# Kernel tuning notes

Measured on AMD Instinct MI355X. Metric: run time of the kernel, lower is better.

## Reference

```python
import jax, jax.numpy as jnp
import numpy as np

B, T, D, H, S = 32, 2048, 512, 64, 3  # batch, time, feature_dim, flow hidden, flow steps
NBLK = 2  # nflows MADE default num_blocks
LOG_2PI = np.float32(np.log(2.0 * np.pi))


def setup_inputs() -> dict:
    key = jax.random.key(0)
    ks = jax.random.split(key, 20)
    rn = lambda k, sh: jax.random.normal(k, sh, dtype=jnp.float32) * 0.05
    return {
        "trend": rn(ks[0], (B, T)),
        "seasonal": rn(ks[1], (B, T)),
        "residual": rn(ks[2], (B, T)),
        # Linear(1, D) for trend / seasonal
        "Wt": rn(ks[3], (D, 1)), "bt": rn(ks[4], (D,)),
        "Ws": rn(ks[5], (D, 1)), "bs": rn(ks[6], (D,)),
        # per-flow-step MADE params (stacked over S steps). With features=1 the
        # masked initial layer contributes only its bias.
        "b_init": rn(ks[7], (S, H)),
        "Wc0": rn(ks[8], (S, H, 1)), "bc0": rn(ks[9], (S, H)),
        # two residual blocks per step: lin1, lin2, context gate
        "W1": rn(ks[10], (S, NBLK, H, H)), "b1": rn(ks[11], (S, NBLK, H)),
        "W2": rn(ks[12], (S, NBLK, H, H)), "b2": rn(ks[13], (S, NBLK, H)),
        "Wcb": rn(ks[14], (S, NBLK, H, 1)), "bcb": rn(ks[15], (S, NBLK, H)),
        # final Linear(H, 2): (unconstrained_scale, shift)
        "Wf": rn(ks[16], (S, 2, H)), "bf": rn(ks[17], (S, 2)),
    }


def _flow_log_prob(x, c, b_init, Wc0, bc0, W1, b1, W2, b2, Wcb, bcb, Wf, bf):
    # x: [N] residual values, c: [N,1] context (previous residual)
    z = x
    logdet = jnp.zeros_like(x)
    for i in range(S):
        h = c @ Wc0[i].T + (bc0[i] + b_init[i])  # [N,H]; input path is fully masked (features=1)
        for j in range(NBLK):  # MaskedResidualBlock
            t = jax.nn.relu(h) @ W1[i, j].T + b1[i, j]
            t = jax.nn.relu(t) @ W2[i, j].T + b2[i, j]
            g = c @ Wcb[i, j].T + bcb[i, j]
            h = h + t * jax.nn.sigmoid(g)  # F.glu(cat(t, g))
        out = jax.nn.relu(h) @ Wf[i].T + bf[i]  # [N,2]
        scale = jax.nn.softplus(out[:, 0]) + 1e-3
        z = scale * z + out[:, 1]
        logdet = logdet + jnp.log(scale)
    return -0.5 * z * z - 0.5 * LOG_2PI + logdet  # StandardNormal.log_prob + logabsdet


def reference(trend, seasonal, residual, Wt, bt, Ws, bs, b_init, Wc0, bc0,
              W1, b1, W2, b2, Wcb, bcb, Wf, bf):
    # Linear(1, D): y = x * W[:,0] + b
    feat_trend = trend[..., None] * Wt[:, 0] + bt      # [B,T,D]
    feat_seasonal = seasonal[..., None] * Ws[:, 0] + bs  # [B,T,D]
    x = residual.reshape(-1)                            # [B*T]
    prev = jnp.concatenate([jnp.zeros_like(residual[:, :1]), residual[:, :-1]], axis=1)
    c = prev.reshape(-1, 1)                             # [B*T,1]
    lp = _flow_log_prob(x, c, b_init, Wc0, bc0, W1, b1, W2, b2, Wcb, bcb, Wf, bf)
    lp = jax.lax.stop_gradient(lp).reshape(B, T, 1)     # torch.no_grad()
    return jnp.concatenate([feat_trend, feat_seasonal, lp], axis=-1)  # [B,T,2D+1]
```

## Files before the change

kernel.cpp:

```cpp
#include <hip/hip_runtime.h>

#define NB 32
#define NT 2048
#define ND 512
#define NH 64
#define NS 3
#define NBLKS 2
#define ROWLEN (2*ND + 1)

typedef __attribute__((ext_vector_type(8))) short bf16x8;
typedef float f32x4 __attribute__((ext_vector_type(4)));

#define W1_OFF 0
#define W2_OFF 24576
#define WF_OFF 49152
#define WS_ELEMS 52224

__device__ __forceinline__ unsigned int f2bf(float f) {
    unsigned int u = __float_as_uint(f);
    return (u + 0x7FFFu + ((u >> 16) & 1u)) >> 16;
}
__device__ __forceinline__ unsigned int pack2(float a, float b) {
    return f2bf(a) | (f2bf(b) << 16);
}

__global__ __launch_bounds__(256) void prepack(
    const float* __restrict__ W1, const float* __restrict__ W2,
    const float* __restrict__ Wf, unsigned short* __restrict__ ws)
{
    int idx = blockIdx.x * 256 + threadIdx.x;
    if (idx < 24576) {
        ws[W1_OFF + idx] = (unsigned short)f2bf(W1[idx]);
    } else if (idx < 49152) {
        int o = idx - 24576;
        ws[W2_OFF + o] = (unsigned short)f2bf(W2[o]);
    } else if (idx < WS_ELEMS) {
        int o = idx - 49152;
        int s = o >> 10, row = (o >> 6) & 15, m = o & 63;
        float v = (row < 2) ? Wf[s * 128 + row * 64 + m] : 0.0f;
        ws[WF_OFF + o] = (unsigned short)f2bf(v);
    }
}

__global__ __launch_bounds__(256, 4) void nf_main(
    const float* __restrict__ trend, const float* __restrict__ seasonal,
    const float* __restrict__ residual,
    const float* __restrict__ Wt, const float* __restrict__ bt,
    const float* __restrict__ Ws, const float* __restrict__ bs,
    const float* __restrict__ b_init, const float* __restrict__ Wc0,
    const float* __restrict__ bc0,
    const float* __restrict__ b1, const float* __restrict__ b2,
    const float* __restrict__ Wcb, const float* __restrict__ bcb,
    const float* __restrict__ bf_, const unsigned short* __restrict__ wpk,
    float* __restrict__ out)
{
    __shared__ float s_tr[64], s_se[64];
    __shared__ unsigned short s_X[4][16][72];

    const int tid  = threadIdx.x;
    const int row0 = blockIdx.x * 64;

    if (tid < 64) { s_tr[tid] = trend[row0 + tid]; s_se[tid] = seasonal[row0 + tid]; }
    __syncthreads();

    {
        float wv[4], bv[4];
        #pragma unroll
        for (int j = 0; j < 4; ++j) {
            int cc = tid + 256 * j;
            if (cc < ND) { wv[j] = Wt[cc];      bv[j] = bt[cc]; }
            else         { wv[j] = Ws[cc - ND]; bv[j] = bs[cc - ND]; }
        }
        for (int rr = 0; rr < 64; ++rr) {
            float a = s_tr[rr], sv = s_se[rr];
            float* rp = out + (size_t)(row0 + rr) * ROWLEN;
            #pragma unroll
            for (int j = 0; j < 4; ++j) {
                int cc = tid + 256 * j;
                rp[cc] = fmaf((cc < ND) ? a : sv, wv[j], bv[j]);
            }
        }
    }

    const int lane = tid & 63;
    const int wv_  = tid >> 6;
    const int r    = lane & 15;
    const int q    = lane >> 4;
    const int n    = row0 + wv_ * 16 + r;
    const float x  = residual[n];
    const float c  = ((n & (NT - 1)) == 0) ? 0.0f : residual[n - 1];
    unsigned short (* const X)[72] = s_X[wv_];
    const int u0 = 4 * q;

    float z = x, logdet = 0.0f;

    for (int i = 0; i < NS; ++i) {
        float h[4][4];
        #pragma unroll
        for (int t = 0; t < 4; ++t) {
            const int ub = i * NH + 16 * t + u0;
            const f32x4 wc  = *(const f32x4*)(Wc0 + ub);
            const f32x4 b0v = *(const f32x4*)(bc0 + ub);
            const f32x4 biv = *(const f32x4*)(b_init + ub);
            #pragma unroll
            for (int e = 0; e < 4; ++e) h[t][e] = fmaf(c, wc[e], b0v[e] + biv[e]);
        }

        for (int j = 0; j < NBLKS; ++j) {
            const int ij = i * NBLKS + j;
            #pragma unroll
            for (int t = 0; t < 4; ++t) {
                uint2 p;
                p.x = pack2(fmaxf(h[t][0], 0.f), fmaxf(h[t][1], 0.f));
                p.y = pack2(fmaxf(h[t][2], 0.f), fmaxf(h[t][3], 0.f));
                *(uint2*)&X[r][16 * t + u0] = p;
            }
            __syncthreads();

            f32x4 D[4];
            {
                const unsigned short* Wb = wpk + W1_OFF + ij * 4096;
                bf16x8 bA = *(const bf16x8*)&X[r][8 * q];
                bf16x8 bB = *(const bf16x8*)&X[r][32 + 8 * q];
                #pragma unroll
                for (int t = 0; t < 4; ++t) {
                    bf16x8 a0 = *(const bf16x8*)&Wb[(16 * t + r) * 64 + 8 * q];
                    bf16x8 a1 = *(const bf16x8*)&Wb[(16 * t + r) * 64 + 32 + 8 * q];
                    f32x4 d = {0.f, 0.f, 0.f, 0.f};
                    d = __builtin_amdgcn_mfma_f32_16x16x32_bf16(a0, bA, d, 0, 0, 0);
                    d = __builtin_amdgcn_mfma_f32_16x16x32_bf16(a1, bB, d, 0, 0, 0);
                    D[t] = d;
                }
            }
            #pragma unroll
            for (int t = 0; t < 4; ++t) {
                const f32x4 bb = *(const f32x4*)(b1 + ij * NH + 16 * t + u0);
                uint2 p;
                p.x = pack2(fmaxf(D[t][0] + bb[0], 0.f), fmaxf(D[t][1] + bb[1], 0.f));
                p.y = pack2(fmaxf(D[t][2] + bb[2], 0.f), fmaxf(D[t][3] + bb[3], 0.f));
                *(uint2*)&X[r][16 * t + u0] = p;
            }
            __syncthreads();

            {
                const unsigned short* Wb = wpk + W2_OFF + ij * 4096;
                bf16x8 bA = *(const bf16x8*)&X[r][8 * q];
                bf16x8 bB = *(const bf16x8*)&X[r][32 + 8 * q];
                #pragma unroll
                for (int t = 0; t < 4; ++t) {
                    bf16x8 a0 = *(const bf16x8*)&Wb[(16 * t + r) * 64 + 8 * q];
                    bf16x8 a1 = *(const bf16x8*)&Wb[(16 * t + r) * 64 + 32 + 8 * q];
                    f32x4 d = {0.f, 0.f, 0.f, 0.f};
                    d = __builtin_amdgcn_mfma_f32_16x16x32_bf16(a0, bA, d, 0, 0, 0);
                    d = __builtin_amdgcn_mfma_f32_16x16x32_bf16(a1, bB, d, 0, 0, 0);
                    D[t] = d;
                }
            }
            #pragma unroll
            for (int t = 0; t < 4; ++t) {
                const int ub = ij * NH + 16 * t + u0;
                const f32x4 b2v = *(const f32x4*)(b2 + ub);
                const f32x4 wg  = *(const f32x4*)(Wcb + ub);
                const f32x4 bg  = *(const f32x4*)(bcb + ub);
                #pragma unroll
                for (int e = 0; e < 4; ++e) {
                    float g  = fmaf(c, wg[e], bg[e]);
                    float sg = 1.0f / (1.0f + __expf(-g));
                    h[t][e] += (D[t][e] + b2v[e]) * sg;
                }
            }
        }

        #pragma unroll
        for (int t = 0; t < 4; ++t) {
            uint2 p;
            p.x = pack2(fmaxf(h[t][0], 0.f), fmaxf(h[t][1], 0.f));
            p.y = pack2(fmaxf(h[t][2], 0.f), fmaxf(h[t][3], 0.f));
            *(uint2*)&X[r][16 * t + u0] = p;
        }
        __syncthreads();
        {
            const unsigned short* Wb = wpk + WF_OFF + i * 1024;
            bf16x8 bA = *(const bf16x8*)&X[r][8 * q];
            bf16x8 bB = *(const bf16x8*)&X[r][32 + 8 * q];
            bf16x8 a0 = *(const bf16x8*)&Wb[r * 64 + 8 * q];
            bf16x8 a1 = *(const bf16x8*)&Wb[r * 64 + 32 + 8 * q];
            f32x4 d = {0.f, 0.f, 0.f, 0.f};
            d = __builtin_amdgcn_mfma_f32_16x16x32_bf16(a0, bA, d, 0, 0, 0);
            d = __builtin_amdgcn_mfma_f32_16x16x32_bf16(a1, bB, d, 0, 0, 0);
            float o0 = d[0] + bf_[2 * i];
            float o1 = d[1] + bf_[2 * i + 1];
            float sp = log1pf(__expf(o0)) + 1e-3f;
            z = fmaf(sp, z, o1);
            logdet += __logf(sp);
        }
        __syncthreads();
    }

    if (q == 0)
        out[(size_t)n * ROWLEN + 2 * ND] = fmaf(-0.5f, z * z, logdet) - 0.91893853320467274178f;
}

extern "C" void kernel_launch(void* const* d_in, const int* in_sizes, int n_in,
                              void* d_out, int out_size, void* d_ws, size_t ws_size,
                              hipStream_t stream) {
    const float* trend    = (const float*)d_in[0];
    const float* seasonal = (const float*)d_in[1];
    const float* residual = (const float*)d_in[2];
    const float* Wt       = (const float*)d_in[3];
    const float* bt       = (const float*)d_in[4];
    const float* Ws       = (const float*)d_in[5];
    const float* bs       = (const float*)d_in[6];
    const float* b_init   = (const float*)d_in[7];
    const float* Wc0      = (const float*)d_in[8];
    const float* bc0      = (const float*)d_in[9];
    const float* W1       = (const float*)d_in[10];
    const float* b1       = (const float*)d_in[11];
    const float* W2       = (const float*)d_in[12];
    const float* b2       = (const float*)d_in[13];
    const float* Wcb      = (const float*)d_in[14];
    const float* bcb      = (const float*)d_in[15];
    const float* Wf       = (const float*)d_in[16];
    const float* bfin     = (const float*)d_in[17];
    float* out            = (float*)d_out;
    unsigned short* wpk   = (unsigned short*)d_ws;

    hipLaunchKernelGGL(prepack, dim3(WS_ELEMS / 256), dim3(256), 0, stream, W1, W2, Wf, wpk);

    const int nrows = NB * NT;
    hipLaunchKernelGGL(nf_main, dim3(nrows / 64), dim3(256), 0, stream,
                       trend, seasonal, residual, Wt, bt, Ws, bs,
                       b_init, Wc0, bc0, b1, b2, Wcb, bcb, bfin, wpk, out);
}
```

Before: 354.3 us.

## Keep MFMA activations in registers via permuted weight rows, drop LDS round-trips

Prepack now permutes the output-unit order of W1 and W2 so that each MFMA's output fragment lands in exactly the lanes and positions the next MFMA needs as its B operand. The activations can then be packed to bf16 directly in registers instead of being written to shared memory and read back. This removes the LDS staging buffer and every __syncthreads in the flow loop, and it also unrolls the block loop. The cost is a more intricate index mapping that must exactly match the MFMA fragment layout, or results will be silently wrong.

```diff
diff --git a/kernel.cpp b/kernel.cpp
--- a/kernel.cpp
+++ b/kernel.cpp
@@ -24,16 +24,22 @@
     return f2bf(a) | (f2bf(b) << 16);
 }
 
+__device__ __forceinline__ int uperm(int s) {
+    return (((s >> 2) & 3) << 3) + (((s >> 4) & 1) << 2) + (s & 3) + ((s >> 5) << 5);
+}
+
 __global__ __launch_bounds__(256) void prepack(
     const float* __restrict__ W1, const float* __restrict__ W2,
     const float* __restrict__ Wf, unsigned short* __restrict__ ws)
 {
     int idx = blockIdx.x * 256 + threadIdx.x;
     if (idx < 24576) {
-        ws[W1_OFF + idx] = (unsigned short)f2bf(W1[idx]);
+        int mat = idx >> 12, s = (idx >> 6) & 63, k = idx & 63;
+        ws[W1_OFF + idx] = (unsigned short)f2bf(W1[(mat << 12) + uperm(s) * 64 + k]);
     } else if (idx < 49152) {
         int o = idx - 24576;
-        ws[W2_OFF + o] = (unsigned short)f2bf(W2[o]);
+        int mat = o >> 12, s = (o >> 6) & 63, k = o & 63;
+        ws[W2_OFF + o] = (unsigned short)f2bf(W2[(mat << 12) + uperm(s) * 64 + k]);
     } else if (idx < WS_ELEMS) {
         int o = idx - 49152;
         int s = o >> 10, row = (o >> 6) & 15, m = o & 63;
@@ -55,7 +61,6 @@
     float* __restrict__ out)
 {
     __shared__ float s_tr[64], s_se[64];
-    __shared__ unsigned short s_X[4][16][72];
 
     const int tid  = threadIdx.x;
     const int row0 = blockIdx.x * 64;
@@ -89,8 +94,11 @@
     const int n    = row0 + wv_ * 16 + r;
     const float x  = residual[n];
     const float c  = ((n & (NT - 1)) == 0) ? 0.0f : residual[n - 1];
-    unsigned short (* const X)[72] = s_X[wv_];
-    const int u0 = 4 * q;
+
+    const int pb0 = 8 * q;
+    const int pbt[4] = {pb0, pb0 + 4, pb0 + 32, pb0 + 36};
+
+    union B8 { unsigned int u[4]; bf16x8 v; };
 
     float z = x, logdet = 0.0f;
 
@@ -98,7 +106,7 @@
         float h[4][4];
         #pragma unroll
         for (int t = 0; t < 4; ++t) {
-            const int ub = i * NH + 16 * t + u0;
+            const int ub = i * NH + pbt[t];
             const f32x4 wc  = *(const f32x4*)(Wc0 + ub);
             const f32x4 b0v = *(const f32x4*)(bc0 + ub);
             const f32x4 biv = *(const f32x4*)(b_init + ub);
@@ -106,59 +114,66 @@
             for (int e = 0; e < 4; ++e) h[t][e] = fmaf(c, wc[e], b0v[e] + biv[e]);
         }
 
+        #pragma unroll
         for (int j = 0; j < NBLKS; ++j) {
             const int ij = i * NBLKS + j;
-            #pragma unroll
-            for (int t = 0; t < 4; ++t) {
-                uint2 p;
-                p.x = pack2(fmaxf(h[t][0], 0.f), fmaxf(h[t][1], 0.f));
-                p.y = pack2(fmaxf(h[t][2], 0.f), fmaxf(h[t][3], 0.f));
-                *(uint2*)&X[r][16 * t + u0] = p;
-            }
-            __syncthreads();
+
+            B8 bA, bB;
+            bA.u[0] = pack2(fmaxf(h[0][0], 0.f), fmaxf(h[0][1], 0.f));
+            bA.u[1] = pack2(fmaxf(h[0][2], 0.f), fmaxf(h[0][3], 0.f));
+            bA.u[2] = pack2(fmaxf(h[1][0], 0.f), fmaxf(h[1][1], 0.f));
+            bA.u[3] = pack2(fmaxf(h[1][2], 0.f), fmaxf(h[1][3], 0.f));
+            bB.u[0] = pack2(fmaxf(h[2][0], 0.f), fmaxf(h[2][1], 0.f));
+            bB.u[1] = pack2(fmaxf(h[2][2], 0.f), fmaxf(h[2][3], 0.f));
+            bB.u[2] = pack2(fmaxf(h[3][0], 0.f), fmaxf(h[3][1], 0.f));
+            bB.u[3] = pack2(fmaxf(h[3][2], 0.f), fmaxf(h[3][3], 0.f));
 
             f32x4 D[4];
             {
                 const unsigned short* Wb = wpk + W1_OFF + ij * 4096;
-                bf16x8 bA = *(const bf16x8*)&X[r][8 * q];
-                bf16x8 bB = *(const bf16x8*)&X[r][32 + 8 * q];
                 #pragma unroll
                 for (int t = 0; t < 4; ++t) {
                     bf16x8 a0 = *(const bf16x8*)&Wb[(16 * t + r) * 64 + 8 * q];
                     bf16x8 a1 = *(const bf16x8*)&Wb[(16 * t + r) * 64 + 32 + 8 * q];
                     f32x4 d = {0.f, 0.f, 0.f, 0.f};
-                    d = __builtin_amdgcn_mfma_f32_16x16x32_bf16(a0, bA, d, 0, 0, 0);
-                    d = __builtin_amdgcn_mfma_f32_16x16x32_bf16(a1, bB, d, 0, 0, 0);
+                    d = __builtin_amdgcn_mfma_f32_16x16x32_bf16(a0, bA.v, d, 0, 0, 0);
+                    d = __builtin_amdgcn_mfma_f32_16x16x32_bf16(a1, bB.v, d, 0, 0, 0);
                     D[t] = d;
                 }
             }
-            #pragma unroll
-            for (int t = 0; t < 4; ++t) {
-                const f32x4 bb = *(const f32x4*)(b1 + ij * NH + 16 * t + u0);
-                uint2 p;
-                p.x = pack2(fmaxf(D[t][0] + bb[0], 0.f), fmaxf(D[t][1] + bb[1], 0.f));
-                p.y = pack2(fmaxf(D[t][2] + bb[2], 0.f), fmaxf(D[t][3] + bb[3], 0.f));
-                *(uint2*)&X[r][16 * t + u0] = p;
-            }
-            __syncthreads();
+
+            B8 cA, cB;
+            {
+                const f32x4 c0 = *(const f32x4*)(b1 + ij * NH + pbt[0]);
+                const f32x4 c1 = *(const f32x4*)(b1 + ij * NH + pbt[1]);
+                const f32x4 c2 = *(const f32x4*)(b1 + ij * NH + pbt[2]);
+                const f32x4 c3 = *(const f32x4*)(b1 + ij * NH + pbt[3]);
+                cA.u[0] = pack2(fmaxf(D[0][0] + c0[0], 0.f), fmaxf(D[0][1] + c0[1], 0.f));
+                cA.u[1] = pack2(fmaxf(D[0][2] + c0[2], 0.f), fmaxf(D[0][3] + c0[3], 0.f));
+                cA.u[2] = pack2(fmaxf(D[1][0] + c1[0], 0.f), fmaxf(D[1][1] + c1[1], 0.f));
+                cA.u[3] = pack2(fmaxf(D[1][2] + c1[2], 0.f), fmaxf(D[1][3] + c1[3], 0.f));
+                cB.u[0] = pack2(fmaxf(D[2][0] + c2[0], 0.f), fmaxf(D[2][1] + c2[1], 0.f));
+                cB.u[1] = pack2(fmaxf(D[2][2] + c2[2], 0.f), fmaxf(D[2][3] + c2[3], 0.f));
+                cB.u[2] = pack2(fmaxf(D[3][0] + c3[0], 0.f), fmaxf(D[3][1] + c3[1], 0.f));
+                cB.u[3] = pack2(fmaxf(D[3][2] + c3[2], 0.f), fmaxf(D[3][3] + c3[3], 0.f));
+            }
 
             {
                 const unsigned short* Wb = wpk + W2_OFF + ij * 4096;
-                bf16x8 bA = *(const bf16x8*)&X[r][8 * q];
-                bf16x8 bB = *(const bf16x8*)&X[r][32 + 8 * q];
                 #pragma unroll
                 for (int t = 0; t < 4; ++t) {
                     bf16x8 a0 = *(const bf16x8*)&Wb[(16 * t + r) * 64 + 8 * q];
                     bf16x8 a1 = *(const bf16x8*)&Wb[(16 * t + r) * 64 + 32 + 8 * q];
                     f32x4 d = {0.f, 0.f, 0.f, 0.f};
-                    d = __builtin_amdgcn_mfma_f32_16x16x32_bf16(a0, bA, d, 0, 0, 0);
-                    d = __builtin_amdgcn_mfma_f32_16x16x32_bf16(a1, bB, d, 0, 0, 0);
+                    d = __builtin_amdgcn_mfma_f32_16x16x32_bf16(a0, cA.v, d, 0, 0, 0);
+                    d = __builtin_amdgcn_mfma_f32_16x16x32_bf16(a1, cB.v, d, 0, 0, 0);
                     D[t] = d;
                 }
             }
+
             #pragma unroll
             for (int t = 0; t < 4; ++t) {
-                const int ub = ij * NH + 16 * t + u0;
+                const int ub = ij * NH + pbt[t];
                 const f32x4 b2v = *(const f32x4*)(b2 + ub);
                 const f32x4 wg  = *(const f32x4*)(Wcb + ub);
                 const f32x4 bg  = *(const f32x4*)(bcb + ub);
@@ -171,30 +186,29 @@
             }
         }
 
-        #pragma unroll
-        for (int t = 0; t < 4; ++t) {
-            uint2 p;
-            p.x = pack2(fmaxf(h[t][0], 0.f), fmaxf(h[t][1], 0.f));
-            p.y = pack2(fmaxf(h[t][2], 0.f), fmaxf(h[t][3], 0.f));
-            *(uint2*)&X[r][16 * t + u0] = p;
-        }
-        __syncthreads();
         {
+            B8 bA, bB;
+            bA.u[0] = pack2(fmaxf(h[0][0], 0.f), fmaxf(h[0][1], 0.f));
+            bA.u[1] = pack2(fmaxf(h[0][2], 0.f), fmaxf(h[0][3], 0.f));
+            bA.u[2] = pack2(fmaxf(h[1][0], 0.f), fmaxf(h[1][1], 0.f));
+            bA.u[3] = pack2(fmaxf(h[1][2], 0.f), fmaxf(h[1][3], 0.f));
+            bB.u[0] = pack2(fmaxf(h[2][0], 0.f), fmaxf(h[2][1], 0.f));
+            bB.u[1] = pack2(fmaxf(h[2][2], 0.f), fmaxf(h[2][3], 0.f));
+            bB.u[2] = pack2(fmaxf(h[3][0], 0.f), fmaxf(h[3][1], 0.f));
+            bB.u[3] = pack2(fmaxf(h[3][2], 0.f), fmaxf(h[3][3], 0.f));
+
             const unsigned short* Wb = wpk + WF_OFF + i * 1024;
-            bf16x8 bA = *(const bf16x8*)&X[r][8 * q];
-            bf16x8 bB = *(const bf16x8*)&X[r][32 + 8 * q];
             bf16x8 a0 = *(const bf16x8*)&Wb[r * 64 + 8 * q];
             bf16x8 a1 = *(const bf16x8*)&Wb[r * 64 + 32 + 8 * q];
             f32x4 d = {0.f, 0.f, 0.f, 0.f};
-            d = __builtin_amdgcn_mfma_f32_16x16x32_bf16(a0, bA, d, 0, 0, 0);
-            d = __builtin_amdgcn_mfma_f32_16x16x32_bf16(a1, bB, d, 0, 0, 0);
+            d = __builtin_amdgcn_mfma_f32_16x16x32_bf16(a0, bA.v, d, 0, 0, 0);
+            d = __builtin_amdgcn_mfma_f32_16x16x32_bf16(a1, bB.v, d, 0, 0, 0);
             float o0 = d[0] + bf_[2 * i];
             float o1 = d[1] + bf_[2 * i + 1];
             float sp = log1pf(__expf(o0)) + 1e-3f;
             z = fmaf(sp, z, o1);
             logdet += __logf(sp);
         }
-        __syncthreads();
     }
 
     if (q == 0)
```

Result: no change. 350.8 us (-1.0%).
